# Optimization experiments

Measured on AMD Instinct MI355X. Metric: run time of the kernel, lower is better.

## Reference

```python
import jax, jax.numpy as jnp
import numpy as np

VLAD_K = 8   # vlad_cluster
GHOST_K = 2  # ghost_cluster
IN_DIM = 512
EPS = 1e-12  # F.normalize eps


def setup_inputs() -> dict:
    key = jax.random.key(0)
    k1, k2, k3, k4 = jax.random.split(key, 4)
    N, C, H, W = 32, IN_DIM, 16, 64
    KG = VLAD_K + GHOST_K
    x = jax.random.normal(k1, (N, C, H, W), dtype=jnp.float32)
    # 1x1 conv weight [KG, C, 1, 1] -> store as [KG, C]; bias [KG]
    conv_w = jax.random.normal(k2, (KG, C), dtype=jnp.float32) * (1.0 / np.sqrt(C))
    conv_b = jax.random.normal(k3, (KG,), dtype=jnp.float32) * 0.01
    centers = jax.random.uniform(k4, (KG, C), dtype=jnp.float32)
    return {"x": x, "conv_w": conv_w, "conv_b": conv_b, "centers": centers}


def reference(x, conv_w, conv_b, centers):
    N, C, H, W = x.shape
    P = H * W
    xf = x.reshape(N, C, P)                                   # [N,C,P]
    # 1x1 conv == per-position matmul over channels
    logits = jnp.einsum('ncp,kc->nkp', xf, conv_w) + conv_b[None, :, None]
    a = jax.nn.softmax(logits, axis=1)                        # softmax over clusters, [N,KG,P]
    # algebraic rewrite of sum_p a*(x - c): (a @ x^T) - (sum_p a) * c
    ax = jnp.einsum('nkp,ncp->nkc', a, xf)                    # [N,KG,C]
    a_sum = a.sum(axis=-1)                                    # [N,KG]
    cluster_res = ax - a_sum[..., None] * centers[None]       # [N,KG,C]
    cluster_res = cluster_res[:, :VLAD_K, :]                  # drop ghost clusters
    norm = jnp.linalg.norm(cluster_res, axis=-1, keepdims=True)
    cluster_res = cluster_res / jnp.maximum(norm, EPS)        # L2 normalize per cluster
    return cluster_res.reshape(N, VLAD_K * C)
```

## Files before the change

kernel.cpp:

```cpp
#include <hip/hip_runtime.h>
#include <math.h>

#define N_   32
#define C_   512
#define P_   1024
#define KG_  10
#define KV_  8
#define PT_  16
#define TILES_ 4
#define PB_  (PT_ * TILES_)
#define NBLK_P 16
#define XS_  513

__global__ __launch_bounds__(256) void vlad_fused(
    const float* __restrict__ x, const float* __restrict__ w,
    const float* __restrict__ bias,
    float* __restrict__ part_ax, float* __restrict__ asum_part) {
  __shared__ __align__(16) float xt[PT_ * XS_];
  __shared__ __align__(16) float part[160 * 20];
  __shared__ __align__(16) float lg[PT_ * KG_];
  __shared__ __align__(16) float a_l[PT_ * KV_];

  const int t    = threadIdx.x;
  const int lane = t & 63;
  const int wv   = t >> 6;
  const int n    = blockIdx.x >> 4;
  const int pb   = blockIdx.x & 15;

  const float* xn = x + (size_t)n * C_ * P_;

  float acc2[2][KV_];
#pragma unroll
  for (int k = 0; k < KV_; ++k) { acc2[0][k] = 0.f; acc2[1][k] = 0.f; }
  float asum[KV_];
#pragma unroll
  for (int k = 0; k < KV_; ++k) asum[k] = 0.f;

  for (int tt = 0; tt < TILES_; ++tt) {
    const int gp = pb * PB_ + tt * PT_;

    __syncthreads();

#pragma unroll
    for (int j = 0; j < 8; ++j) {
      const int lid = j * 256 + t;
      const int c   = lid >> 2;
      const int p4  = (lid & 3) * 4;
      const float4 v =
          *reinterpret_cast<const float4*>(xn + (size_t)c * P_ + gp + p4);
      xt[(p4 + 0) * XS_ + c] = v.x;
      xt[(p4 + 1) * XS_ + c] = v.y;
      xt[(p4 + 2) * XS_ + c] = v.z;
      xt[(p4 + 3) * XS_ + c] = v.w;
    }
    __syncthreads();

    float acc[4][KG_];
#pragma unroll
    for (int pj = 0; pj < 4; ++pj)
#pragma unroll
      for (int k = 0; k < KG_; ++k) acc[pj][k] = 0.f;

#pragma unroll 2
    for (int cb = 0; cb < 8; ++cb) {
      const int c = cb * 64 + lane;
      float wreg[KG_];
#pragma unroll
      for (int k = 0; k < KG_; ++k) wreg[k] = w[k * C_ + c];
#pragma unroll
      for (int pj = 0; pj < 4; ++pj) {
        const float xv = xt[(wv * 4 + pj) * XS_ + c];
#pragma unroll
        for (int k = 0; k < KG_; ++k) acc[pj][k] += xv * wreg[k];
      }
    }
#pragma unroll
    for (int pj = 0; pj < 4; ++pj) {
#pragma unroll
      for (int k = 0; k < KG_; ++k) {
        float v = acc[pj][k];
        v += __shfl_xor(v, 1, 64);
        v += __shfl_xor(v, 2, 64);
        if ((lane & 3) == 0)
          part[(wv * 40 + pj * 10 + k) * 20 + (lane >> 2)] = v;
      }
    }
    __syncthreads();

    if (t < 160) {
      const float* row = &part[t * 20];
      const float4 s0 = *reinterpret_cast<const float4*>(row);
      const float4 s1 = *reinterpret_cast<const float4*>(row + 4);
      const float4 s2 = *reinterpret_cast<const float4*>(row + 8);
      const float4 s3 = *reinterpret_cast<const float4*>(row + 12);
      const float s = ((s0.x + s0.y) + (s0.z + s0.w)) +
                      ((s1.x + s1.y) + (s1.z + s1.w)) +
                      ((s2.x + s2.y) + (s2.z + s2.w)) +
                      ((s3.x + s3.y) + (s3.z + s3.w));
      const int k = t % 10;
      const int p = (t / 40) * 4 + (t % 40) / 10;
      lg[p * KG_ + k] = s + bias[k];
    }
    __syncthreads();

    if (t < PT_) {
      float l[KG_];
      float m = -1e30f;
#pragma unroll
      for (int k = 0; k < KG_; ++k) {
        l[k] = lg[t * KG_ + k];
        m = fmaxf(m, l[k]);
      }
      float sum = 0.f;
#pragma unroll
      for (int k = 0; k < KG_; ++k) { l[k] = __expf(l[k] - m); sum += l[k]; }
      const float inv = 1.f / sum;
#pragma unroll
      for (int k = 0; k < KV_; ++k) {
        const float a = l[k] * inv;
        a_l[t * KV_ + k] = a;
        float s = a;
        s += __shfl_xor(s, 1, 64);
        s += __shfl_xor(s, 2, 64);
        s += __shfl_xor(s, 4, 64);
        s += __shfl_xor(s, 8, 64);
        asum[k] += s;
      }
    }
    __syncthreads();

#pragma unroll 4
    for (int p = 0; p < PT_; ++p) {
      const float4 a0 = *reinterpret_cast<const float4*>(&a_l[p * KV_]);
      const float4 a1 = *reinterpret_cast<const float4*>(&a_l[p * KV_ + 4]);
      const float x0 = xt[p * XS_ + t];
      const float x1 = xt[p * XS_ + t + 256];
      acc2[0][0] += a0.x * x0;  acc2[1][0] += a0.x * x1;
      acc2[0][1] += a0.y * x0;  acc2[1][1] += a0.y * x1;
      acc2[0][2] += a0.z * x0;  acc2[1][2] += a0.z * x1;
      acc2[0][3] += a0.w * x0;  acc2[1][3] += a0.w * x1;
      acc2[0][4] += a1.x * x0;  acc2[1][4] += a1.x * x1;
      acc2[0][5] += a1.y * x0;  acc2[1][5] += a1.y * x1;
      acc2[0][6] += a1.z * x0;  acc2[1][6] += a1.z * x1;
      acc2[0][7] += a1.w * x0;  acc2[1][7] += a1.w * x1;
    }
  }

  const size_t base = (size_t)(n * NBLK_P + pb) * KV_ * C_;
#pragma unroll
  for (int k = 0; k < KV_; ++k) {
    part_ax[base + k * C_ + t]       = acc2[0][k];
    part_ax[base + k * C_ + t + 256] = acc2[1][k];
  }
  if (t == 0) {
#pragma unroll
    for (int k = 0; k < KV_; ++k)
      asum_part[(n * NBLK_P + pb) * KV_ + k] = asum[k];
  }
}

__global__ __launch_bounds__(256) void vlad_reduce(
    const float* __restrict__ part_ax, const float* __restrict__ asum_part,
    const float* __restrict__ centers, float* __restrict__ out) {
  __shared__ float sred[4];
  const int n = blockIdx.x >> 3;
  const int k = blockIdx.x & 7;
  const int t = threadIdx.x, lane = t & 63, wv = t >> 6;

  float s0 = 0.f, s1 = 0.f, asv = 0.f;
#pragma unroll
  for (int b = 0; b < NBLK_P; ++b) {
    const size_t base = ((size_t)(n * NBLK_P + b) * KV_ + k) * C_;
    s0  += part_ax[base + t];
    s1  += part_ax[base + t + 256];
    asv += asum_part[(n * NBLK_P + b) * KV_ + k];
  }
  const float r0 = s0 - asv * centers[k * C_ + t];
  const float r1 = s1 - asv * centers[k * C_ + t + 256];

  float ss = r0 * r0 + r1 * r1;
#pragma unroll
  for (int d = 1; d < 64; d <<= 1) ss += __shfl_xor(ss, d, 64);
  if (lane == 0) sred[wv] = ss;
  __syncthreads();
  const float tot = (sred[0] + sred[1]) + (sred[2] + sred[3]);
  const float inv = 1.f / fmaxf(sqrtf(tot), 1e-12f);

  out[(size_t)n * (KV_ * C_) + k * C_ + t]       = r0 * inv;
  out[(size_t)n * (KV_ * C_) + k * C_ + t + 256] = r1 * inv;
}

extern "C" void kernel_launch(void* const* d_in, const int* in_sizes, int n_in,
                              void* d_out, int out_size, void* d_ws, size_t ws_size,
                              hipStream_t stream) {
  const float* x       = (const float*)d_in[0];
  const float* conv_w  = (const float*)d_in[1];
  const float* conv_b  = (const float*)d_in[2];
  const float* centers = (const float*)d_in[3];
  float* out = (float*)d_out;

  float* part_ax   = (float*)d_ws;
  float* asum_part = part_ax + (size_t)N_ * NBLK_P * KV_ * C_;

  hipLaunchKernelGGL(vlad_fused, dim3(N_ * NBLK_P), dim3(256), 0, stream,
                     x, conv_w, conv_b, part_ax, asum_part);
  hipLaunchKernelGGL(vlad_reduce, dim3(N_ * KV_), dim3(256), 0, stream,
                     part_ax, asum_part, centers, out);
}
```

Measured before the change: 126.6 us.

## Prefetch next x tile into registers, stage conv weights in LDS with float4 reads

Loads the next point tile of x into registers while the current tile is being computed, so global loads overlap with compute. Conv weights are staged once in shared memory, and the logits loop now reads float4 vectors of x and w, which changes the partial-sum reduction layout (8-lane shuffle, 8 partials per row). Row padding moves from 513 to 516 to keep rows float4-aligned, and __syncthreads is replaced by an LDS-only waitcnt plus s_barrier. In exchange it uses more registers (prefetch buffer) and more LDS, and the 516 padding may bring back bank conflicts on the transposed stores.

```diff
diff --git a/kernel.cpp b/kernel.cpp
--- a/kernel.cpp
+++ b/kernel.cpp
@@ -10,14 +10,19 @@
 #define TILES_ 4
 #define PB_  (PT_ * TILES_)
 #define NBLK_P 16
-#define XS_  513
+#define XS_  516
+
+__device__ __forceinline__ void bar_lds() {
+  asm volatile("s_waitcnt lgkmcnt(0)\n\ts_barrier" ::: "memory");
+}
 
 __global__ __launch_bounds__(256) void vlad_fused(
     const float* __restrict__ x, const float* __restrict__ w,
     const float* __restrict__ bias,
     float* __restrict__ part_ax, float* __restrict__ asum_part) {
   __shared__ __align__(16) float xt[PT_ * XS_];
-  __shared__ __align__(16) float part[160 * 20];
+  __shared__ __align__(16) float wt[KG_ * C_];
+  __shared__ __align__(16) float part[160 * 12];
   __shared__ __align__(16) float lg[PT_ * KG_];
   __shared__ __align__(16) float a_l[PT_ * KV_];
 
@@ -26,8 +31,27 @@
   const int wv   = t >> 6;
   const int n    = blockIdx.x >> 4;
   const int pb   = blockIdx.x & 15;
+  const int gp0  = pb * PB_;
 
   const float* xn = x + (size_t)n * C_ * P_;
+
+  float4 wstage[5];
+#pragma unroll
+  for (int j = 0; j < 5; ++j)
+    wstage[j] = *reinterpret_cast<const float4*>(w + (j * 256 + t) * 4);
+
+  float4 pf[8];
+  {
+    const int c  = t >> 2;
+    const int p4 = (t & 3) * 4;
+#pragma unroll
+    for (int j = 0; j < 8; ++j)
+      pf[j] = *reinterpret_cast<const float4*>(
+          xn + (size_t)(j * 64 + c) * P_ + gp0 + p4);
+  }
+#pragma unroll
+  for (int j = 0; j < 5; ++j)
+    *reinterpret_cast<float4*>(&wt[(j * 256 + t) * 4]) = wstage[j];
 
   float acc2[2][KV_];
 #pragma unroll
@@ -36,24 +60,29 @@
 #pragma unroll
   for (int k = 0; k < KV_; ++k) asum[k] = 0.f;
 
+  const int cT  = t >> 2;
+  const int p4T = (t & 3) * 4;
+
   for (int tt = 0; tt < TILES_; ++tt) {
-    const int gp = pb * PB_ + tt * PT_;
-
-    __syncthreads();
+    if (tt) bar_lds();
 
 #pragma unroll
     for (int j = 0; j < 8; ++j) {
-      const int lid = j * 256 + t;
-      const int c   = lid >> 2;
-      const int p4  = (lid & 3) * 4;
-      const float4 v =
-          *reinterpret_cast<const float4*>(xn + (size_t)c * P_ + gp + p4);
-      xt[(p4 + 0) * XS_ + c] = v.x;
-      xt[(p4 + 1) * XS_ + c] = v.y;
-      xt[(p4 + 2) * XS_ + c] = v.z;
-      xt[(p4 + 3) * XS_ + c] = v.w;
-    }
-    __syncthreads();
+      const int c = j * 64 + cT;
+      xt[(p4T + 0) * XS_ + c] = pf[j].x;
+      xt[(p4T + 1) * XS_ + c] = pf[j].y;
+      xt[(p4T + 2) * XS_ + c] = pf[j].z;
+      xt[(p4T + 3) * XS_ + c] = pf[j].w;
+    }
+    bar_lds();
+
+    if (tt + 1 < TILES_) {
+      const int gp = gp0 + (tt + 1) * PT_;
+#pragma unroll
+      for (int j = 0; j < 8; ++j)
+        pf[j] = *reinterpret_cast<const float4*>(
+            xn + (size_t)(j * 64 + cT) * P_ + gp + p4T);
+    }
 
     float acc[4][KG_];
 #pragma unroll
@@ -61,17 +90,21 @@
 #pragma unroll
       for (int k = 0; k < KG_; ++k) acc[pj][k] = 0.f;
 
-#pragma unroll 2
-    for (int cb = 0; cb < 8; ++cb) {
-      const int c = cb * 64 + lane;
-      float wreg[KG_];
-#pragma unroll
-      for (int k = 0; k < KG_; ++k) wreg[k] = w[k * C_ + c];
+#pragma unroll
+    for (int half = 0; half < 2; ++half) {
+      const int c0 = half * 256 + lane * 4;
+      float4 wk[KG_];
+#pragma unroll
+      for (int k = 0; k < KG_; ++k)
+        wk[k] = *reinterpret_cast<const float4*>(&wt[k * C_ + c0]);
 #pragma unroll
       for (int pj = 0; pj < 4; ++pj) {
-        const float xv = xt[(wv * 4 + pj) * XS_ + c];
-#pragma unroll
-        for (int k = 0; k < KG_; ++k) acc[pj][k] += xv * wreg[k];
+        const float4 x4 =
+            *reinterpret_cast<const float4*>(&xt[(wv * 4 + pj) * XS_ + c0]);
+#pragma unroll
+        for (int k = 0; k < KG_; ++k)
+          acc[pj][k] += x4.x * wk[k].x + x4.y * wk[k].y
+                      + x4.z * wk[k].z + x4.w * wk[k].w;
       }
     }
 #pragma unroll
@@ -81,27 +114,24 @@
         float v = acc[pj][k];
         v += __shfl_xor(v, 1, 64);
         v += __shfl_xor(v, 2, 64);
-        if ((lane & 3) == 0)
-          part[(wv * 40 + pj * 10 + k) * 20 + (lane >> 2)] = v;
-      }
-    }
-    __syncthreads();
+        v += __shfl_xor(v, 4, 64);
+        if ((lane & 7) == 0)
+          part[(wv * 40 + pj * 10 + k) * 12 + (lane >> 3)] = v;
+      }
+    }
+    bar_lds();
 
     if (t < 160) {
-      const float* row = &part[t * 20];
+      const float* row = &part[t * 12];
       const float4 s0 = *reinterpret_cast<const float4*>(row);
       const float4 s1 = *reinterpret_cast<const float4*>(row + 4);
-      const float4 s2 = *reinterpret_cast<const float4*>(row + 8);
-      const float4 s3 = *reinterpret_cast<const float4*>(row + 12);
       const float s = ((s0.x + s0.y) + (s0.z + s0.w)) +
-                      ((s1.x + s1.y) + (s1.z + s1.w)) +
-                      ((s2.x + s2.y) + (s2.z + s2.w)) +
-                      ((s3.x + s3.y) + (s3.z + s3.w));
+                      ((s1.x + s1.y) + (s1.z + s1.w));
       const int k = t % 10;
       const int p = (t / 40) * 4 + (t % 40) / 10;
       lg[p * KG_ + k] = s + bias[k];
     }
-    __syncthreads();
+    bar_lds();
 
     if (t < PT_) {
       float l[KG_];
@@ -127,7 +157,7 @@
         asum[k] += s;
       }
     }
-    __syncthreads();
+    bar_lds();
 
 #pragma unroll 4
     for (int p = 0; p < PT_; ++p) {
```

Result: slower. 129.6 us (+2.3%).
